# Performance work log

Hardware: AMD Instinct MI355X
Metric: run time of the kernel (lower is better)

The kernel has to match this reference:

```python
import jax, jax.numpy as jnp
import numpy as np

B, S = 4096, 64
L, W = 16, 8          # fixed letter image size in the module
K = 3                 # kernel size
OL, OW = L - K + 1, W - K + 1  # 14, 6 (valid conv, stride 1)


def setup_inputs() -> dict:
    key = jax.random.key(0)
    k1, k2 = jax.random.split(key)
    x = jax.random.normal(k1, (B, S, L * W), dtype=jnp.float32)
    kernel = jax.random.normal(k2, (K, K), dtype=jnp.float32)
    return {"x": x, "kernel": kernel}


def reference(x, kernel):
    # x: [B, S, 128] -> images [B*S, 1, 16, 8]
    imgs = x.reshape(B * S, 1, L, W)
    kern = kernel.reshape(1, 1, K, K)  # OIHW
    out = jax.lax.conv_general_dilated(
        imgs, kern,
        window_strides=(1, 1), padding="VALID",
        dimension_numbers=("NCHW", "OIHW", "NCHW"),
    )  # [B*S, 1, 14, 6]
    out = out.reshape(B, S, OL * OW)
    return jax.nn.relu(out)
```

## Files before the change

### kernel.cpp

```cpp
#include <hip/hip_runtime.h>


#define BLOCK 256
#define IPB   64
#define STRIDE 132
#define NIMG_TOTAL (4096 * 64)

__global__ __launch_bounds__(BLOCK, 4) void conv3x3_relu_kernel(
    const float* __restrict__ x,
    const float* __restrict__ kern,
    float* __restrict__ out)
{
    __shared__ float s[IPB * STRIDE];

    const int tid = threadIdx.x;
    const long long img0 = (long long)blockIdx.x * IPB;

    const float k00 = kern[0], k01 = kern[1], k02 = kern[2];
    const float k10 = kern[3], k11 = kern[4], k12 = kern[5];
    const float k20 = kern[6], k21 = kern[7], k22 = kern[8];

    const float4* src = reinterpret_cast<const float4*>(x + img0 * 128);
    #pragma unroll
    for (int it = 0; it < 8; ++it) {
        const int f    = it * BLOCK + tid;
        const int img  = f >> 5;
        const int off4 = f & 31;
        const float4 v = src[f];
        *reinterpret_cast<float4*>(&s[img * STRIDE + off4 * 4]) = v;
    }
    __syncthreads();

    const int img  = tid >> 2;
    const int tq   = tid & 3;
    const int rs   = (tq < 2) ? (tq * 4) : (8 + (tq - 2) * 3);
    const int rcnt = (tq < 2) ? 4 : 3;
    const float* ip = &s[img * STRIDE];

    float acc[4][6];
    #pragma unroll
    for (int rr = 0; rr < 4; ++rr) {
        if (rr < rcnt) {
            const int r = rs + rr;
            float w0[8], w1[8], w2[8];
            *reinterpret_cast<float4*>(&w0[0]) = *reinterpret_cast<const float4*>(ip + r * 8);
            *reinterpret_cast<float4*>(&w0[4]) = *reinterpret_cast<const float4*>(ip + r * 8 + 4);
            *reinterpret_cast<float4*>(&w1[0]) = *reinterpret_cast<const float4*>(ip + r * 8 + 8);
            *reinterpret_cast<float4*>(&w1[4]) = *reinterpret_cast<const float4*>(ip + r * 8 + 12);
            *reinterpret_cast<float4*>(&w2[0]) = *reinterpret_cast<const float4*>(ip + r * 8 + 16);
            *reinterpret_cast<float4*>(&w2[4]) = *reinterpret_cast<const float4*>(ip + r * 8 + 20);
            #pragma unroll
            for (int c = 0; c < 6; ++c) {
                float a = w0[c] * k00 + w0[c + 1] * k01 + w0[c + 2] * k02
                        + w1[c] * k10 + w1[c + 1] * k11 + w1[c + 2] * k12
                        + w2[c] * k20 + w2[c + 1] * k21 + w2[c + 2] * k22;
                acc[rr][c] = fmaxf(a, 0.0f);
            }
        }
    }
    __syncthreads();

    #pragma unroll
    for (int rr = 0; rr < 4; ++rr) {
        if (rr < rcnt) {
            float* op = &s[img * 84 + (rs + rr) * 6];
            *reinterpret_cast<float2*>(op)     = make_float2(acc[rr][0], acc[rr][1]);
            *reinterpret_cast<float2*>(op + 2) = make_float2(acc[rr][2], acc[rr][3]);
            *reinterpret_cast<float2*>(op + 4) = make_float2(acc[rr][4], acc[rr][5]);
        }
    }
    __syncthreads();

    float4* dst = reinterpret_cast<float4*>(out + img0 * 84);
    const float4* s4 = reinterpret_cast<const float4*>(s);
    #pragma unroll
    for (int it = 0; it < 6; ++it) {
        const int f = it * BLOCK + tid;
        if (f < (IPB * 84) / 4) dst[f] = s4[f];
    }
}

extern "C" void kernel_launch(void* const* d_in, const int* in_sizes, int n_in,
                              void* d_out, int out_size, void* d_ws, size_t ws_size,
                              hipStream_t stream) {
    const float* x    = (const float*)d_in[0];
    const float* kern = (const float*)d_in[1];
    float* out        = (float*)d_out;
    const int nblocks = NIMG_TOTAL / IPB;
    conv3x3_relu_kernel<<<nblocks, BLOCK, 0, stream>>>(x, kern, out);
}
```

Before: 216.1 us.

## Process multiple image chunks per block with register-prefetched global loads

Each block now loops over four 64-image chunks. It stages the next chunk's global loads in registers while the current chunk is computed and written out, so memory latency overlaps with compute. Input rows are also reused in a rolling three-row window, which cuts shared-memory reads. The trade-off is higher register use for the prefetch buffers and a grid one quarter the size, which may lower occupancy and latency hiding.

```diff
diff --git a/kernel.cpp b/kernel.cpp
--- a/kernel.cpp
+++ b/kernel.cpp
@@ -4,6 +4,7 @@
 #define BLOCK 256
 #define IPB   64
 #define STRIDE 132
+#define NC    4
 #define NIMG_TOTAL (4096 * 64)
 
 __global__ __launch_bounds__(BLOCK, 4) void conv3x3_relu_kernel(
@@ -14,69 +15,93 @@
     __shared__ float s[IPB * STRIDE];
 
     const int tid = threadIdx.x;
-    const long long img0 = (long long)blockIdx.x * IPB;
-
     const float k00 = kern[0], k01 = kern[1], k02 = kern[2];
     const float k10 = kern[3], k11 = kern[4], k12 = kern[5];
     const float k20 = kern[6], k21 = kern[7], k22 = kern[8];
-
-    const float4* src = reinterpret_cast<const float4*>(x + img0 * 128);
-    #pragma unroll
-    for (int it = 0; it < 8; ++it) {
-        const int f    = it * BLOCK + tid;
-        const int img  = f >> 5;
-        const int off4 = f & 31;
-        const float4 v = src[f];
-        *reinterpret_cast<float4*>(&s[img * STRIDE + off4 * 4]) = v;
-    }
-    __syncthreads();
 
     const int img  = tid >> 2;
     const int tq   = tid & 3;
     const int rs   = (tq < 2) ? (tq * 4) : (8 + (tq - 2) * 3);
     const int rcnt = (tq < 2) ? 4 : 3;
-    const float* ip = &s[img * STRIDE];
 
-    float acc[4][6];
+    const long long base_img = (long long)blockIdx.x * (IPB * NC);
+
+    float4 pf[2][8];
+
+    {
+        const float4* src = reinterpret_cast<const float4*>(x + base_img * 128);
+        #pragma unroll
+        for (int it = 0; it < 8; ++it) pf[0][it] = src[it * BLOCK + tid];
+    }
+
     #pragma unroll
-    for (int rr = 0; rr < 4; ++rr) {
-        if (rr < rcnt) {
-            const int r = rs + rr;
-            float w0[8], w1[8], w2[8];
-            *reinterpret_cast<float4*>(&w0[0]) = *reinterpret_cast<const float4*>(ip + r * 8);
-            *reinterpret_cast<float4*>(&w0[4]) = *reinterpret_cast<const float4*>(ip + r * 8 + 4);
-            *reinterpret_cast<float4*>(&w1[0]) = *reinterpret_cast<const float4*>(ip + r * 8 + 8);
-            *reinterpret_cast<float4*>(&w1[4]) = *reinterpret_cast<const float4*>(ip + r * 8 + 12);
-            *reinterpret_cast<float4*>(&w2[0]) = *reinterpret_cast<const float4*>(ip + r * 8 + 16);
-            *reinterpret_cast<float4*>(&w2[4]) = *reinterpret_cast<const float4*>(ip + r * 8 + 20);
+    for (int t = 0; t < NC; ++t) {
+        if (t > 0) __syncthreads();
+
+        #pragma unroll
+        for (int it = 0; it < 8; ++it) {
+            const int f  = it * BLOCK + tid;
+            const int im = f >> 5;
+            const int o4 = f & 31;
+            *reinterpret_cast<float4*>(&s[im * STRIDE + o4 * 4]) = pf[t & 1][it];
+        }
+
+        if (t + 1 < NC) {
+            const float4* src = reinterpret_cast<const float4*>(
+                x + (base_img + (long long)(t + 1) * IPB) * 128);
             #pragma unroll
-            for (int c = 0; c < 6; ++c) {
-                float a = w0[c] * k00 + w0[c + 1] * k01 + w0[c + 2] * k02
-                        + w1[c] * k10 + w1[c + 1] * k11 + w1[c + 2] * k12
-                        + w2[c] * k20 + w2[c + 1] * k21 + w2[c + 2] * k22;
-                acc[rr][c] = fmaxf(a, 0.0f);
+            for (int it = 0; it < 8; ++it) pf[(t + 1) & 1][it] = src[it * BLOCK + tid];
+        }
+        __syncthreads();
+
+        const float* ip = &s[img * STRIDE];
+        float w[3][8];
+        float acc[4][6];
+        *reinterpret_cast<float4*>(&w[0][0]) = *reinterpret_cast<const float4*>(ip + rs * 8);
+        *reinterpret_cast<float4*>(&w[0][4]) = *reinterpret_cast<const float4*>(ip + rs * 8 + 4);
+        *reinterpret_cast<float4*>(&w[1][0]) = *reinterpret_cast<const float4*>(ip + (rs + 1) * 8);
+        *reinterpret_cast<float4*>(&w[1][4]) = *reinterpret_cast<const float4*>(ip + (rs + 1) * 8 + 4);
+        #pragma unroll
+        for (int rr = 0; rr < 4; ++rr) {
+            if (rr < rcnt) {
+                float* wn = w[(rr + 2) % 3];
+                *reinterpret_cast<float4*>(&wn[0]) =
+                    *reinterpret_cast<const float4*>(ip + (rs + rr + 2) * 8);
+                *reinterpret_cast<float4*>(&wn[4]) =
+                    *reinterpret_cast<const float4*>(ip + (rs + rr + 2) * 8 + 4);
+                const float* r0 = w[rr % 3];
+                const float* r1 = w[(rr + 1) % 3];
+                const float* r2 = wn;
+                #pragma unroll
+                for (int c = 0; c < 6; ++c) {
+                    float a = r0[c] * k00 + r0[c + 1] * k01 + r0[c + 2] * k02
+                            + r1[c] * k10 + r1[c + 1] * k11 + r1[c + 2] * k12
+                            + r2[c] * k20 + r2[c + 1] * k21 + r2[c + 2] * k22;
+                    acc[rr][c] = fmaxf(a, 0.0f);
+                }
             }
         }
-    }
-    __syncthreads();
+        __syncthreads();
 
-    #pragma unroll
-    for (int rr = 0; rr < 4; ++rr) {
-        if (rr < rcnt) {
-            float* op = &s[img * 84 + (rs + rr) * 6];
-            *reinterpret_cast<float2*>(op)     = make_float2(acc[rr][0], acc[rr][1]);
-            *reinterpret_cast<float2*>(op + 2) = make_float2(acc[rr][2], acc[rr][3]);
-            *reinterpret_cast<float2*>(op + 4) = make_float2(acc[rr][4], acc[rr][5]);
+        #pragma unroll
+        for (int rr = 0; rr < 4; ++rr) {
+            if (rr < rcnt) {
+                float* op = &s[img * 84 + (rs + rr) * 6];
+                *reinterpret_cast<float2*>(op)     = make_float2(acc[rr][0], acc[rr][1]);
+                *reinterpret_cast<float2*>(op + 2) = make_float2(acc[rr][2], acc[rr][3]);
+                *reinterpret_cast<float2*>(op + 4) = make_float2(acc[rr][4], acc[rr][5]);
+            }
         }
-    }
-    __syncthreads();
+        __syncthreads();
 
-    float4* dst = reinterpret_cast<float4*>(out + img0 * 84);
-    const float4* s4 = reinterpret_cast<const float4*>(s);
-    #pragma unroll
-    for (int it = 0; it < 6; ++it) {
-        const int f = it * BLOCK + tid;
-        if (f < (IPB * 84) / 4) dst[f] = s4[f];
+        float4* dst = reinterpret_cast<float4*>(
+            out + (base_img + (long long)t * IPB) * 84);
+        const float4* s4 = reinterpret_cast<const float4*>(s);
+        #pragma unroll
+        for (int it = 0; it < 6; ++it) {
+            const int f = it * BLOCK + tid;
+            if (f < (IPB * 84) / 4) dst[f] = s4[f];
+        }
     }
 }
 
@@ -86,6 +111,6 @@
     const float* x    = (const float*)d_in[0];
     const float* kern = (const float*)d_in[1];
     float* out        = (float*)d_out;
-    const int nblocks = NIMG_TOTAL / IPB;
+    const int nblocks = NIMG_TOTAL / (IPB * NC);
     conv3x3_relu_kernel<<<nblocks, BLOCK, 0, stream>>>(x, kern, out);
 }
```

Result: slower. 241.8 us (+11.9%).

## Replace LDS staging with register-resident rows and lane shuffles for halo

Applied to the files above, without the earlier changes.

Each group of 8 lanes now handles one image, with each lane loading two rows directly from global memory into registers. The two halo rows each lane needs come from its neighbour lane via shuffles, replacing the shared-memory staging, the three barriers and the LDS round-trip for output. Loads and stores use nontemporal builtins to avoid cache pollution on this streaming pattern. In exchange, the last lane of each group idles on the store, and global accesses are 64-byte strided per instruction rather than fully contiguous.

```diff
diff --git a/kernel.cpp b/kernel.cpp
--- a/kernel.cpp
+++ b/kernel.cpp
@@ -2,81 +2,62 @@
 
 
 #define BLOCK 256
-#define IPB   64
-#define STRIDE 132
 #define NIMG_TOTAL (4096 * 64)
 
-__global__ __launch_bounds__(BLOCK, 4) void conv3x3_relu_kernel(
+typedef float f32x4 __attribute__((ext_vector_type(4)));
+
+__global__ __launch_bounds__(BLOCK) void conv3x3_relu_kernel(
     const float* __restrict__ x,
     const float* __restrict__ kern,
     float* __restrict__ out)
 {
-    __shared__ float s[IPB * STRIDE];
-
-    const int tid = threadIdx.x;
-    const long long img0 = (long long)blockIdx.x * IPB;
+    const int tid   = threadIdx.x;
+    const int lane8 = tid & 7;
+    const long long img = (long long)blockIdx.x * (BLOCK / 8) + (tid >> 3);
 
     const float k00 = kern[0], k01 = kern[1], k02 = kern[2];
     const float k10 = kern[3], k11 = kern[4], k12 = kern[5];
     const float k20 = kern[6], k21 = kern[7], k22 = kern[8];
 
-    const float4* src = reinterpret_cast<const float4*>(x + img0 * 128);
-    #pragma unroll
-    for (int it = 0; it < 8; ++it) {
-        const int f    = it * BLOCK + tid;
-        const int img  = f >> 5;
-        const int off4 = f & 31;
-        const float4 v = src[f];
-        *reinterpret_cast<float4*>(&s[img * STRIDE + off4 * 4]) = v;
-    }
-    __syncthreads();
+    const f32x4* src = reinterpret_cast<const f32x4*>(x + img * 128) + lane8 * 4;
+    f32x4 v0 = __builtin_nontemporal_load(&src[0]);
+    f32x4 v1 = __builtin_nontemporal_load(&src[1]);
+    f32x4 v2 = __builtin_nontemporal_load(&src[2]);
+    f32x4 v3 = __builtin_nontemporal_load(&src[3]);
 
-    const int img  = tid >> 2;
-    const int tq   = tid & 3;
-    const int rs   = (tq < 2) ? (tq * 4) : (8 + (tq - 2) * 3);
-    const int rcnt = (tq < 2) ? 4 : 3;
-    const float* ip = &s[img * STRIDE];
-
-    float acc[4][6];
-    #pragma unroll
-    for (int rr = 0; rr < 4; ++rr) {
-        if (rr < rcnt) {
-            const int r = rs + rr;
-            float w0[8], w1[8], w2[8];
-            *reinterpret_cast<float4*>(&w0[0]) = *reinterpret_cast<const float4*>(ip + r * 8);
-            *reinterpret_cast<float4*>(&w0[4]) = *reinterpret_cast<const float4*>(ip + r * 8 + 4);
-            *reinterpret_cast<float4*>(&w1[0]) = *reinterpret_cast<const float4*>(ip + r * 8 + 8);
-            *reinterpret_cast<float4*>(&w1[4]) = *reinterpret_cast<const float4*>(ip + r * 8 + 12);
-            *reinterpret_cast<float4*>(&w2[0]) = *reinterpret_cast<const float4*>(ip + r * 8 + 16);
-            *reinterpret_cast<float4*>(&w2[4]) = *reinterpret_cast<const float4*>(ip + r * 8 + 20);
-            #pragma unroll
-            for (int c = 0; c < 6; ++c) {
-                float a = w0[c] * k00 + w0[c + 1] * k01 + w0[c + 2] * k02
-                        + w1[c] * k10 + w1[c + 1] * k11 + w1[c + 2] * k12
-                        + w2[c] * k20 + w2[c + 1] * k21 + w2[c + 2] * k22;
-                acc[rr][c] = fmaxf(a, 0.0f);
-            }
-        }
-    }
-    __syncthreads();
+    float own0[8], own1[8], nbr0[8], nbr1[8];
+    *reinterpret_cast<f32x4*>(&own0[0]) = v0;
+    *reinterpret_cast<f32x4*>(&own0[4]) = v1;
+    *reinterpret_cast<f32x4*>(&own1[0]) = v2;
+    *reinterpret_cast<f32x4*>(&own1[4]) = v3;
 
     #pragma unroll
-    for (int rr = 0; rr < 4; ++rr) {
-        if (rr < rcnt) {
-            float* op = &s[img * 84 + (rs + rr) * 6];
-            *reinterpret_cast<float2*>(op)     = make_float2(acc[rr][0], acc[rr][1]);
-            *reinterpret_cast<float2*>(op + 2) = make_float2(acc[rr][2], acc[rr][3]);
-            *reinterpret_cast<float2*>(op + 4) = make_float2(acc[rr][4], acc[rr][5]);
-        }
+    for (int j = 0; j < 8; ++j) nbr0[j] = __shfl_down(own0[j], 1);
+    #pragma unroll
+    for (int j = 0; j < 8; ++j) nbr1[j] = __shfl_down(own1[j], 1);
+
+    float a0[6], a1[6];
+    #pragma unroll
+    for (int c = 0; c < 6; ++c) {
+        float s0 = own0[c] * k00 + own0[c + 1] * k01 + own0[c + 2] * k02
+                 + own1[c] * k10 + own1[c + 1] * k11 + own1[c + 2] * k12
+                 + nbr0[c] * k20 + nbr0[c + 1] * k21 + nbr0[c + 2] * k22;
+        float s1 = own1[c] * k00 + own1[c + 1] * k01 + own1[c + 2] * k02
+                 + nbr0[c] * k10 + nbr0[c + 1] * k11 + nbr0[c + 2] * k12
+                 + nbr1[c] * k20 + nbr1[c + 1] * k21 + nbr1[c + 2] * k22;
+        a0[c] = fmaxf(s0, 0.0f);
+        a1[c] = fmaxf(s1, 0.0f);
     }
-    __syncthreads();
 
-    float4* dst = reinterpret_cast<float4*>(out + img0 * 84);
-    const float4* s4 = reinterpret_cast<const float4*>(s);
-    #pragma unroll
-    for (int it = 0; it < 6; ++it) {
-        const int f = it * BLOCK + tid;
-        if (f < (IPB * 84) / 4) dst[f] = s4[f];
+    if (lane8 < 7) {
+        f32x4 w0, w1, w2;
+        w0.x = a0[0]; w0.y = a0[1]; w0.z = a0[2]; w0.w = a0[3];
+        w1.x = a0[4]; w1.y = a0[5]; w1.z = a1[0]; w1.w = a1[1];
+        w2.x = a1[2]; w2.y = a1[3]; w2.z = a1[4]; w2.w = a1[5];
+        f32x4* dst = reinterpret_cast<f32x4*>(out + img * 84 + lane8 * 12);
+        __builtin_nontemporal_store(w0, &dst[0]);
+        __builtin_nontemporal_store(w1, &dst[1]);
+        __builtin_nontemporal_store(w2, &dst[2]);
     }
 }
 
@@ -86,6 +67,6 @@
     const float* x    = (const float*)d_in[0];
     const float* kern = (const float*)d_in[1];
     float* out        = (float*)d_out;
-    const int nblocks = NIMG_TOTAL / IPB;
+    const int nblocks = NIMG_TOTAL / (BLOCK / 8);
     conv3x3_relu_kernel<<<nblocks, BLOCK, 0, stream>>>(x, kern, out);
 }
```

After: 226.4 us. +4.7%, slower.
